# Kernel tuning notes

Hardware: AMD Instinct MI355X
Metric: run time of the kernel (lower is better)

## Reference

```python
import jax, jax.numpy as jnp
from jax import lax
import numpy as np

INPUT_SCALE = 1.0
RES_SCALE = 1.0
RES_SIZE = 2048
INPUT_SIZE = 512
SEQ_LEN = 8192


def setup_inputs() -> dict:
    key = jax.random.key(0)
    k1, k2, k3, k4 = jax.random.split(key, 4)
    inp = jax.random.normal(k1, (SEQ_LEN, INPUT_SIZE), dtype=jnp.float32)
    state = jax.random.normal(k2, (RES_SIZE,), dtype=jnp.float32)
    W_in = jax.random.normal(k3, (RES_SIZE, INPUT_SIZE), dtype=jnp.float32)
    W_res = jax.random.normal(k4, (RES_SIZE, RES_SIZE), dtype=jnp.float32)
    return {"input": inp, "state": state, "W_in": W_in, "W_res": W_res}


def reference(input, state, W_in, W_res):
    # states[i+1] = tanh(input_scale * W_in @ input[i] + res_scale * W_res @ states[i]) / sqrt(res_size)
    inv_sqrt_n = jnp.asarray(1.0 / np.sqrt(RES_SIZE), dtype=input.dtype)
    # hoist all input projections into one GEMM: (seq_len, res_size)
    u = (INPUT_SCALE * input) @ W_in.T

    def step(s, u_t):
        s_new = jnp.tanh(u_t + RES_SCALE * (W_res @ s)) * inv_sqrt_n
        return s_new, s_new

    _, states = lax.scan(step, state, u)
    # prepend the initial state -> (seq_len+1, res_size)
    return jnp.concatenate([state[None, :], states], axis=0)
```

## Files before the change

### kernel.cpp

```cpp
#include <hip/hip_runtime.h>

#define T_SEQ   8192
#define N_RES   2048
#define K_IN    512

#define G_BLOCKS 64
#define B_THREADS 512
#define ROWS_PER_WAVE 4
#define ROWS_PER_BLOCK 32
static_assert(G_BLOCKS * ROWS_PER_BLOCK == N_RES, "row partition mismatch");

#define INV_SQRT_N 0.022097086912079612f

#define ENC_OFF 0.1f
#define ENC_THR 0.05f

typedef unsigned long long u64;
typedef unsigned int u32;
typedef float f32x2 __attribute__((ext_vector_type(2)));

__device__ __forceinline__ float fast_tanh(float v) {
    float e = __expf(2.0f * v);
    return 1.0f - 2.0f / (e + 1.0f);
}

#define KEEP2(v) asm("" : "+v"(v))

__global__ __launch_bounds__(B_THREADS, 2)
void reservoir_v9(const float* __restrict__ input,
                  const float* __restrict__ state0,
                  const float* __restrict__ W_in,
                  const float* __restrict__ W_res,
                  float* __restrict__ out,
                  u64* __restrict__ ring)
{
    const int tid  = threadIdx.x;
    const int lane = tid & 63;
    const int wave = tid >> 6;
    const int blk  = blockIdx.x;
    const int r0   = blk * ROWS_PER_BLOCK + wave * ROWS_PER_WAVE;

    __shared__ float s_lds[2][N_RES];

    f32x2 wr2[ROWS_PER_WAVE][16];
    f32x2 wi2[ROWS_PER_WAVE][4];
    #pragma unroll
    for (int k = 0; k < ROWS_PER_WAVE; ++k) {
        const float* rrow = W_res + (size_t)(r0 + k) * N_RES;
        #pragma unroll
        for (int i = 0; i < 8; ++i) {
            float4 w = *reinterpret_cast<const float4*>(rrow + 4 * lane + 256 * i);
            wr2[k][2 * i]     = (f32x2){w.x, w.y};
            wr2[k][2 * i + 1] = (f32x2){w.z, w.w};
        }
        const float* irow = W_in + (size_t)(r0 + k) * K_IN;
        #pragma unroll
        for (int i = 0; i < 2; ++i) {
            float4 w = *reinterpret_cast<const float4*>(irow + 4 * lane + 256 * i);
            wi2[k][2 * i]     = (f32x2){w.x, w.y};
            wi2[k][2 * i + 1] = (f32x2){w.z, w.w};
        }
    }

    if (blk == 0)
        for (int j = tid; j < N_RES; j += B_THREADS) out[j] = state0[j];

    #pragma unroll
    for (int i = 0; i < 4; ++i)
        s_lds[0][i * 512 + tid] = state0[i * 512 + tid];

    f32x2 xv[4];
    {
        float4 a = *reinterpret_cast<const float4*>(input + 4 * lane);
        float4 b = *reinterpret_cast<const float4*>(input + 4 * lane + 256);
        xv[0] = (f32x2){a.x, a.y}; xv[1] = (f32x2){a.z, a.w};
        xv[2] = (f32x2){b.x, b.y}; xv[3] = (f32x2){b.z, b.w};
    }

    for (int t = 0; t < T_SEQ; ++t) {
        const int buf = t & 1;

        f32x2 xn[4] = {xv[0], xv[1], xv[2], xv[3]};
        if (t + 1 < T_SEQ) {
            const float* xr = input + (size_t)(t + 1) * K_IN;
            float4 a = *reinterpret_cast<const float4*>(xr + 4 * lane);
            float4 b = *reinterpret_cast<const float4*>(xr + 4 * lane + 256);
            xn[0] = (f32x2){a.x, a.y}; xn[1] = (f32x2){a.z, a.w};
            xn[2] = (f32x2){b.x, b.y}; xn[3] = (f32x2){b.z, b.w};
        }

        if (t > 0) {
            const u64* rp = ring + (buf << 10);
            const float phi = ((t >> 1) & 1) ? -1.0f : 1.0f;
            float2 sv2[2];
            u32 pend = 0x3u;
            while (pend) {
                #pragma unroll
                for (int i = 0; i < 2; ++i) {
                    if (pend & (1u << i)) {
                        u64 e = __hip_atomic_load(rp + i * 512 + tid,
                                                  __ATOMIC_RELAXED, __HIP_MEMORY_SCOPE_AGENT);
                        float lo = __uint_as_float((u32)e);
                        float hi = __uint_as_float((u32)(e >> 32));
                        if (phi * lo > ENC_THR && phi * hi > ENC_THR) {
                            sv2[i] = make_float2(fmaf(phi, lo, -ENC_OFF),
                                                 fmaf(phi, hi, -ENC_OFF));
                            pend &= ~(1u << i);
                        }
                    }
                }
                if (pend) __builtin_amdgcn_s_sleep(1);
            }
            #pragma unroll
            for (int i = 0; i < 2; ++i)
                *reinterpret_cast<float2*>(&s_lds[buf][2 * (i * 512 + tid)]) = sv2[i];
        }
        __syncthreads();

        f32x2 sp[16];
        #pragma unroll
        for (int i = 0; i < 8; ++i) {
            float4 s = *reinterpret_cast<const float4*>(&s_lds[buf][4 * lane + 256 * i]);
            sp[2 * i]     = (f32x2){s.x, s.y};
            sp[2 * i + 1] = (f32x2){s.z, s.w};
        }

        f32x2 acc2[ROWS_PER_WAVE];
        #pragma unroll
        for (int k = 0; k < ROWS_PER_WAVE; ++k) {
            f32x2 a = (f32x2){0.0f, 0.0f};
            #pragma unroll
            for (int i = 0; i < 4; ++i)
                a = __builtin_elementwise_fma(wi2[k][i], xv[i], a);
            #pragma unroll
            for (int i = 0; i < 16; ++i)
                a = __builtin_elementwise_fma(wr2[k][i], sp[i], a);
            acc2[k] = a;
        }

        float acc[ROWS_PER_WAVE];
        #pragma unroll
        for (int k = 0; k < ROWS_PER_WAVE; ++k) acc[k] = acc2[k].x + acc2[k].y;
        #pragma unroll
        for (int off = 32; off > 0; off >>= 1) {
            #pragma unroll
            for (int k = 0; k < ROWS_PER_WAVE; ++k)
                acc[k] += __shfl_xor(acc[k], off, 64);
        }

        const float v0 = fast_tanh(acc[0]) * INV_SQRT_N;
        const float v1 = fast_tanh(acc[1]) * INV_SQRT_N;
        const float v2 = fast_tanh(acc[2]) * INV_SQRT_N;
        const float v3 = fast_tanh(acc[3]) * INV_SQRT_N;
        const int   slotn = (t + 1) & 1;
        const float phin  = (((t + 1) >> 1) & 1) ? -1.0f : 1.0f;
        if (lane == 0) {
            u64 pk = (u64)__float_as_uint(phin * (v0 + ENC_OFF)) |
                     ((u64)__float_as_uint(phin * (v1 + ENC_OFF)) << 32);
            __hip_atomic_store(ring + (slotn << 10) + (r0 >> 1), pk,
                               __ATOMIC_RELAXED, __HIP_MEMORY_SCOPE_AGENT);
        } else if (lane == 1) {
            u64 pk = (u64)__float_as_uint(phin * (v2 + ENC_OFF)) |
                     ((u64)__float_as_uint(phin * (v3 + ENC_OFF)) << 32);
            __hip_atomic_store(ring + (slotn << 10) + (r0 >> 1) + 1, pk,
                               __ATOMIC_RELAXED, __HIP_MEMORY_SCOPE_AGENT);
        } else if (lane == 2) {
            *reinterpret_cast<float4*>(out + (size_t)(t + 1) * N_RES + r0) =
                make_float4(v0, v1, v2, v3);
        }

        #pragma unroll
        for (int k = 0; k < ROWS_PER_WAVE; ++k) {
            #pragma unroll
            for (int i = 0; i < 16; ++i) KEEP2(wr2[k][i]);
            #pragma unroll
            for (int i = 0; i < 4; ++i)  KEEP2(wi2[k][i]);
        }

        #pragma unroll
        for (int i = 0; i < 4; ++i) xv[i] = xn[i];
    }
}

extern "C" void kernel_launch(void* const* d_in, const int* in_sizes, int n_in,
                              void* d_out, int out_size, void* d_ws, size_t ws_size,
                              hipStream_t stream) {
    const float* input  = (const float*)d_in[0];
    const float* state0 = (const float*)d_in[1];
    const float* W_in   = (const float*)d_in[2];
    const float* W_res  = (const float*)d_in[3];
    float* out = (float*)d_out;
    u64* ring  = (u64*)d_ws;

    hipMemsetAsync(d_ws, 0, 2 * (N_RES / 2) * sizeof(u64), stream);

    void* args[] = { (void*)&input, (void*)&state0, (void*)&W_in, (void*)&W_res,
                     (void*)&out, (void*)&ring };
    hipLaunchCooperativeKernel((const void*)reservoir_v9,
                               dim3(G_BLOCKS), dim3(B_THREADS),
                               args, 0, stream);
}
```

Measured before the change: 18.84 ms.

## Drop LDS staging and barrier; each wave polls full state from ring

Each wave now reads the whole previous state vector directly from the global ring, 16 u64 slots per lane in a permuted layout, and folds values into its FMAs as they arrive. This removes the shared-memory double buffer and the per-step __syncthreads, so waves no longer wait on each other within a block. The cost is eight times more global or L2 polling traffic per block, and a remapped W_res register layout and ring slot permutation to match the new lane ownership.

```diff
diff --git a/kernel.cpp b/kernel.cpp
--- a/kernel.cpp
+++ b/kernel.cpp
@@ -15,6 +15,8 @@
 #define ENC_OFF 0.1f
 #define ENC_THR 0.05f
 
+#define SLOT(p) ((((p) & 15) << 6) | ((p) >> 4))
+
 typedef unsigned long long u64;
 typedef unsigned int u32;
 typedef float f32x2 __attribute__((ext_vector_type(2)));
@@ -27,12 +29,12 @@
 #define KEEP2(v) asm("" : "+v"(v))
 
 __global__ __launch_bounds__(B_THREADS, 2)
-void reservoir_v9(const float* __restrict__ input,
-                  const float* __restrict__ state0,
-                  const float* __restrict__ W_in,
-                  const float* __restrict__ W_res,
-                  float* __restrict__ out,
-                  u64* __restrict__ ring)
+void reservoir_v10(const float* __restrict__ input,
+                   const float* __restrict__ state0,
+                   const float* __restrict__ W_in,
+                   const float* __restrict__ W_res,
+                   float* __restrict__ out,
+                   u64* __restrict__ ring)
 {
     const int tid  = threadIdx.x;
     const int lane = tid & 63;
@@ -40,16 +42,14 @@
     const int blk  = blockIdx.x;
     const int r0   = blk * ROWS_PER_BLOCK + wave * ROWS_PER_WAVE;
 
-    __shared__ float s_lds[2][N_RES];
-
     f32x2 wr2[ROWS_PER_WAVE][16];
     f32x2 wi2[ROWS_PER_WAVE][4];
     #pragma unroll
     for (int k = 0; k < ROWS_PER_WAVE; ++k) {
-        const float* rrow = W_res + (size_t)(r0 + k) * N_RES;
+        const float* rrow = W_res + (size_t)(r0 + k) * N_RES + 32 * lane;
         #pragma unroll
         for (int i = 0; i < 8; ++i) {
-            float4 w = *reinterpret_cast<const float4*>(rrow + 4 * lane + 256 * i);
+            float4 w = *reinterpret_cast<const float4*>(rrow + 4 * i);
             wr2[k][2 * i]     = (f32x2){w.x, w.y};
             wr2[k][2 * i + 1] = (f32x2){w.z, w.w};
         }
@@ -64,10 +64,6 @@
 
     if (blk == 0)
         for (int j = tid; j < N_RES; j += B_THREADS) out[j] = state0[j];
-
-    #pragma unroll
-    for (int i = 0; i < 4; ++i)
-        s_lds[0][i * 512 + tid] = state0[i * 512 + tid];
 
     f32x2 xv[4];
     {
@@ -78,8 +74,6 @@
     }
 
     for (int t = 0; t < T_SEQ; ++t) {
-        const int buf = t & 1;
-
         f32x2 xn[4] = {xv[0], xv[1], xv[2], xv[3]};
         if (t + 1 < T_SEQ) {
             const float* xr = input + (size_t)(t + 1) * K_IN;
@@ -89,53 +83,57 @@
             xn[2] = (f32x2){b.x, b.y}; xn[3] = (f32x2){b.z, b.w};
         }
 
-        if (t > 0) {
-            const u64* rp = ring + (buf << 10);
+        f32x2 acc2[ROWS_PER_WAVE];
+        #pragma unroll
+        for (int k = 0; k < ROWS_PER_WAVE; ++k) {
+            f32x2 a = (f32x2){0.0f, 0.0f};
+            #pragma unroll
+            for (int i = 0; i < 4; ++i)
+                a = __builtin_elementwise_fma(wi2[k][i], xv[i], a);
+            acc2[k] = a;
+        }
+
+        if (t == 0) {
+            const float* sp = state0 + 32 * lane;
+            #pragma unroll
+            for (int i = 0; i < 8; ++i) {
+                float4 s = *reinterpret_cast<const float4*>(sp + 4 * i);
+                f32x2 s01 = (f32x2){s.x, s.y}, s23 = (f32x2){s.z, s.w};
+                #pragma unroll
+                for (int k = 0; k < ROWS_PER_WAVE; ++k) {
+                    acc2[k] = __builtin_elementwise_fma(wr2[k][2 * i],     s01, acc2[k]);
+                    acc2[k] = __builtin_elementwise_fma(wr2[k][2 * i + 1], s23, acc2[k]);
+                }
+            }
+        } else {
             const float phi = ((t >> 1) & 1) ? -1.0f : 1.0f;
-            float2 sv2[2];
-            u32 pend = 0x3u;
+            const u64* rp = ring + ((t & 1) << 10) + lane;
+            u32 pend = 0xFFFFu;
             while (pend) {
+                u64 e[16];
                 #pragma unroll
-                for (int i = 0; i < 2; ++i) {
+                for (int i = 0; i < 16; ++i)
+                    if (pend & (1u << i))
+                        e[i] = __hip_atomic_load(rp + 64 * i, __ATOMIC_RELAXED,
+                                                 __HIP_MEMORY_SCOPE_AGENT);
+                #pragma unroll
+                for (int i = 0; i < 16; ++i) {
                     if (pend & (1u << i)) {
-                        u64 e = __hip_atomic_load(rp + i * 512 + tid,
-                                                  __ATOMIC_RELAXED, __HIP_MEMORY_SCOPE_AGENT);
-                        float lo = __uint_as_float((u32)e);
-                        float hi = __uint_as_float((u32)(e >> 32));
+                        float lo = __uint_as_float((u32)e[i]);
+                        float hi = __uint_as_float((u32)(e[i] >> 32));
                         if (phi * lo > ENC_THR && phi * hi > ENC_THR) {
-                            sv2[i] = make_float2(fmaf(phi, lo, -ENC_OFF),
-                                                 fmaf(phi, hi, -ENC_OFF));
+                            f32x2 sv = {fmaf(phi, lo, -ENC_OFF),
+                                        fmaf(phi, hi, -ENC_OFF)};
+                            #pragma unroll
+                            for (int k = 0; k < ROWS_PER_WAVE; ++k)
+                                acc2[k] = __builtin_elementwise_fma(wr2[k][i], sv,
+                                                                    acc2[k]);
                             pend &= ~(1u << i);
                         }
                     }
                 }
                 if (pend) __builtin_amdgcn_s_sleep(1);
             }
-            #pragma unroll
-            for (int i = 0; i < 2; ++i)
-                *reinterpret_cast<float2*>(&s_lds[buf][2 * (i * 512 + tid)]) = sv2[i];
-        }
-        __syncthreads();
-
-        f32x2 sp[16];
-        #pragma unroll
-        for (int i = 0; i < 8; ++i) {
-            float4 s = *reinterpret_cast<const float4*>(&s_lds[buf][4 * lane + 256 * i]);
-            sp[2 * i]     = (f32x2){s.x, s.y};
-            sp[2 * i + 1] = (f32x2){s.z, s.w};
-        }
-
-        f32x2 acc2[ROWS_PER_WAVE];
-        #pragma unroll
-        for (int k = 0; k < ROWS_PER_WAVE; ++k) {
-            f32x2 a = (f32x2){0.0f, 0.0f};
-            #pragma unroll
-            for (int i = 0; i < 4; ++i)
-                a = __builtin_elementwise_fma(wi2[k][i], xv[i], a);
-            #pragma unroll
-            for (int i = 0; i < 16; ++i)
-                a = __builtin_elementwise_fma(wr2[k][i], sp[i], a);
-            acc2[k] = a;
         }
 
         float acc[ROWS_PER_WAVE];
@@ -154,15 +152,16 @@
         const float v3 = fast_tanh(acc[3]) * INV_SQRT_N;
         const int   slotn = (t + 1) & 1;
         const float phin  = (((t + 1) >> 1) & 1) ? -1.0f : 1.0f;
+        const int   p0    = r0 >> 1;
         if (lane == 0) {
             u64 pk = (u64)__float_as_uint(phin * (v0 + ENC_OFF)) |
                      ((u64)__float_as_uint(phin * (v1 + ENC_OFF)) << 32);
-            __hip_atomic_store(ring + (slotn << 10) + (r0 >> 1), pk,
+            __hip_atomic_store(ring + (slotn << 10) + SLOT(p0), pk,
                                __ATOMIC_RELAXED, __HIP_MEMORY_SCOPE_AGENT);
         } else if (lane == 1) {
             u64 pk = (u64)__float_as_uint(phin * (v2 + ENC_OFF)) |
                      ((u64)__float_as_uint(phin * (v3 + ENC_OFF)) << 32);
-            __hip_atomic_store(ring + (slotn << 10) + (r0 >> 1) + 1, pk,
+            __hip_atomic_store(ring + (slotn << 10) + SLOT(p0 + 1), pk,
                                __ATOMIC_RELAXED, __HIP_MEMORY_SCOPE_AGENT);
         } else if (lane == 2) {
             *reinterpret_cast<float4*>(out + (size_t)(t + 1) * N_RES + r0) =
@@ -196,7 +195,7 @@
 
     void* args[] = { (void*)&input, (void*)&state0, (void*)&W_in, (void*)&W_res,
                      (void*)&out, (void*)&ring };
-    hipLaunchCooperativeKernel((const void*)reservoir_v9,
+    hipLaunchCooperativeKernel((const void*)reservoir_v10,
                                dim3(G_BLOCKS), dim3(B_THREADS),
                                args, 0, stream);
 }
```

Measured after the change: 57.45 ms. +205.0%, slower.
